# Optimization experiments

Measured on AMD Instinct MI355X. Metric: run time of the kernel, lower is better.

## Reference

```python
import jax, jax.numpy as jnp
import numpy as np

TEMPERATURE = 0.1
BATCH_SIZE = 64
EPS = 1e-8  # torch.nn.CosineSimilarity eps
NEG_INF = -1e30

B, C, D = 64, 16, 512  # batch, children per sample, feature dim


def setup_inputs() -> dict:
    key = jax.random.key(0)
    k1, k2, k3, k4 = jax.random.split(key, 4)
    children_is = jax.random.normal(k1, (B, C, D), dtype=jnp.float32)
    children_js = jax.random.normal(k2, (B, C, D), dtype=jnp.float32)
    partnet_ids = jnp.arange(B, dtype=jnp.int64 if jax.config.jax_enable_x64 else jnp.int32)
    neg_idx_j = jax.random.randint(k3, (B, B, C), 0, C)  # negatives drawn from children_js
    neg_idx_k = jax.random.randint(k4, (B, B, C), 0, C)  # negatives drawn from children_is
    return {
        "children_is": children_is,
        "children_js": children_js,
        "partnet_ids": partnet_ids,
        "neg_idx_j": neg_idx_j,
        "neg_idx_k": neg_idx_k,
    }


def _safe_norm(x, axis=-1):
    return jnp.maximum(jnp.sqrt(jnp.sum(x * x, axis=axis)), EPS)


def _ntxent(ci, cj, pids, nj, nk):
    b = ci.shape[0]
    fi = ci.reshape(b, -1)  # [B, L] flattened anchors
    fj = cj.reshape(b, -1)  # [B, L] flattened positives
    norm_i = _safe_norm(fi)

    # positive: cos(flat(children_i), flat(children_j[i])) / T
    pos = jnp.sum(fi * fj, axis=-1) / (norm_i * _safe_norm(fj))  # [B]

    src = jnp.arange(b)[None, :, None]  # broadcast source-sample index
    # gathered negatives: g*[i, j] = children_*[j, neg_idx[i, j]] flattened -> [B, B, L]
    gj = cj[src, nj].reshape(b, b, -1)
    gk = ci[src, nk].reshape(b, b, -1)

    sim_j = jnp.einsum('il,ijl->ij', fi, gj) / (norm_i[:, None] * _safe_norm(gj))
    sim_k = jnp.einsum('il,ijl->ij', fi, gk) / (norm_i[:, None] * _safe_norm(gk))

    # negative pair valid iff j != i and partnet ids differ
    eye = jnp.arange(b)
    mask = (eye[None, :] != eye[:, None]) & (pids[None, :] != pids[:, None])  # [B, B]

    logits = jnp.concatenate(
        [pos[:, None],
         jnp.where(mask, sim_j, NEG_INF),
         jnp.where(mask, sim_k, NEG_INF)], axis=1) / TEMPERATURE  # [B, 1+2B]

    # CrossEntropy with label 0, reduction='sum' over the batch of anchors
    loss = jnp.sum(-logits[:, 0] + jax.scipy.special.logsumexp(logits, axis=1))
    return loss / (2.0 * BATCH_SIZE)


def reference(children_is, children_js, partnet_ids, neg_idx_j, neg_idx_k):
    return _ntxent(children_is, children_js, partnet_ids, neg_idx_j, neg_idx_k)
```

## Files before the change

kernel.cpp:

```cpp
#include <hip/hip_runtime.h>
#include <math.h>

#define BB 64
#define CC 16
#define DD 512
#define LL 8192
#define EPSV 1e-8f
#define INVT 10.0f
#define NEGINF_T (-1e31f)

#define WS_N2I 0
#define WS_N2J 1024
#define WS_DJ  2048
#define WS_DK  6144
#define WS_POS 10240

__device__ __forceinline__ float dot4(float4 a, float4 b) {
    return a.x * b.x + a.y * b.y + a.z * b.z + a.w * b.w;
}

__device__ __forceinline__ float wave_reduce(float v) {
    #pragma unroll
    for (int off = 32; off; off >>= 1) v += __shfl_down(v, off);
    return v;
}

__global__ __launch_bounds__(256) void ntx_main(const float* __restrict__ ci,
                                                const float* __restrict__ cj,
                                                const int* __restrict__ nj,
                                                const int* __restrict__ nk,
                                                float* __restrict__ ws,
                                                float* __restrict__ out) {
    const int b = blockIdx.x, tid = threadIdx.x;

    if (b < 1024) {
        const int jt = b & 15;
        const int i  = b >> 4;

        const float4* fi4 = (const float4*)(ci + i * LL);
        float4 fiv[8];
        #pragma unroll
        for (int it = 0; it < 8; ++it) fiv[it] = fi4[tid + 256 * it];

        const int d4   = tid & 127;
        const int half = tid >> 7;
        const float4* cj4 = (const float4*)cj;
        const float4* ci4 = (const float4*)ci;

        float aj[4] = {0.f, 0.f, 0.f, 0.f};
        float ak[4] = {0.f, 0.f, 0.f, 0.f};

        #pragma unroll
        for (int it = 0; it < 8; ++it) {
            const int c = half + 2 * it;
            #pragma unroll
            for (int jj = 0; jj < 4; ++jj) {
                const int j = jt * 4 + jj;
                const int ib = (i * BB + j) * CC + c;
                const int idxj = __builtin_amdgcn_readfirstlane(nj[ib]);
                const int idxk = __builtin_amdgcn_readfirstlane(nk[ib]);
                float4 vj = cj4[(j * CC + idxj) * 128 + d4];
                float4 vk = ci4[(j * CC + idxk) * 128 + d4];
                aj[jj] += dot4(fiv[it], vj);
                ak[jj] += dot4(fiv[it], vk);
            }
        }

        __shared__ float red[4][2][4];
        #pragma unroll
        for (int jj = 0; jj < 4; ++jj) {
            float rj = wave_reduce(aj[jj]);
            float rk = wave_reduce(ak[jj]);
            if ((tid & 63) == 0) { red[jj][0][tid >> 6] = rj; red[jj][1][tid >> 6] = rk; }
        }
        __syncthreads();
        if (tid < 8) {
            const int jj = tid >> 1, side = tid & 1;
            float s = red[jj][side][0] + red[jj][side][1] + red[jj][side][2] + red[jj][side][3];
            ws[(side ? WS_DK : WS_DJ) + i * BB + jt * 4 + jj] = s;
        }
    } else if (b < 1536) {
        const int row  = (b - 1024) * 4 + (tid >> 6);
        const int lane = tid & 63;
        const int r    = row & 1023;
        const float4* src = (const float4*)(row < 1024 ? ci : cj);
        float4 v1 = src[r * 128 + lane];
        float4 v2 = src[r * 128 + 64 + lane];
        float acc = dot4(v1, v1) + dot4(v2, v2);
        acc = wave_reduce(acc);
        if (lane == 0) ws[(row < 1024 ? WS_N2I : WS_N2J) + r] = acc;
    } else {
        __shared__ float red2[4];
        const int i = b - 1536;
        if (b == 1536 && tid == 0) out[0] = 0.f;
        const float4* fi = (const float4*)(ci + i * LL);
        const float4* fj = (const float4*)(cj + i * LL);
        float acc = 0.f;
        #pragma unroll
        for (int it = 0; it < 8; ++it) acc += dot4(fi[tid + 256 * it], fj[tid + 256 * it]);
        acc = wave_reduce(acc);
        if ((tid & 63) == 0) red2[tid >> 6] = acc;
        __syncthreads();
        if (tid == 0) ws[WS_POS + i] = red2[0] + red2[1] + red2[2] + red2[3];
    }
}

__global__ __launch_bounds__(64) void ntx_final(const int* __restrict__ pids,
                                                const int* __restrict__ nj,
                                                const int* __restrict__ nk,
                                                const float* __restrict__ ws,
                                                float* __restrict__ out) {
    const int i = blockIdx.x, j = threadIdx.x;
    __shared__ float sn2i[1024], sn2j[1024];
    const float4* n2i4 = (const float4*)(ws + WS_N2I);
    const float4* n2j4 = (const float4*)(ws + WS_N2J);
    #pragma unroll
    for (int t = 0; t < 4; ++t) {
        ((float4*)sn2i)[j + 64 * t] = n2i4[j + 64 * t];
        ((float4*)sn2j)[j + 64 * t] = n2j4[j + 64 * t];
    }
    __syncthreads();

    float si = 0.f, sjf = 0.f;
    #pragma unroll
    for (int c = 0; c < CC; ++c) { si += sn2i[i * CC + c]; sjf += sn2j[i * CC + c]; }
    const float ni = fmaxf(sqrtf(si), EPSV);
    const float l0 = ws[WS_POS + i] / (ni * fmaxf(sqrtf(sjf), EPSV)) * INVT;

    const int4* nj4 = (const int4*)(nj + (i * BB + j) * CC);
    const int4* nk4 = (const int4*)(nk + (i * BB + j) * CC);
    float gj = 0.f, gk = 0.f;
    #pragma unroll
    for (int t = 0; t < 4; ++t) {
        int4 a = nj4[t];
        gj += sn2j[j * CC + a.x] + sn2j[j * CC + a.y] + sn2j[j * CC + a.z] + sn2j[j * CC + a.w];
        int4 bq = nk4[t];
        gk += sn2i[j * CC + bq.x] + sn2i[j * CC + bq.y] + sn2i[j * CC + bq.z] + sn2i[j * CC + bq.w];
    }

    const bool valid = (j != i) && (pids[j] != pids[i]);
    float lj = NEGINF_T, lk = NEGINF_T;
    if (valid) {
        const float inv = INVT / ni;
        lj = ws[WS_DJ + i * BB + j] / fmaxf(sqrtf(gj), EPSV) * inv;
        lk = ws[WS_DK + i * BB + j] / fmaxf(sqrtf(gk), EPSV) * inv;
    }

    float m = fmaxf(lj, lk);
    #pragma unroll
    for (int off = 32; off; off >>= 1) m = fmaxf(m, __shfl_xor(m, off));
    m = fmaxf(m, l0);

    float s = __expf(lj - m) + __expf(lk - m);
    s = wave_reduce(s);
    if (j == 0) {
        s += __expf(l0 - m);
        const float loss_i = -l0 + m + __logf(s);
        atomicAdd(out, loss_i * (1.0f / (2.0f * BB)));
    }
}

extern "C" void kernel_launch(void* const* d_in, const int* in_sizes, int n_in,
                              void* d_out, int out_size, void* d_ws, size_t ws_size,
                              hipStream_t stream) {
    const float* ci  = (const float*)d_in[0];
    const float* cj  = (const float*)d_in[1];
    const int*  pids = (const int*) d_in[2];
    const int*  nj   = (const int*) d_in[3];
    const int*  nk   = (const int*) d_in[4];
    float* ws  = (float*)d_ws;
    float* out = (float*)d_out;

    ntx_main<<<1600, 256, 0, stream>>>(ci, cj, nj, nk, ws, out);
    ntx_final<<<BB, 64, 0, stream>>>(pids, nj, nk, ws, out);
}
```

Baseline: 88.70 us.

## Stage source-sample rows in shared memory and tile anchors per block

```diff
diff --git a/kernel.cpp b/kernel.cpp
--- a/kernel.cpp
+++ b/kernel.cpp
@@ -31,77 +31,83 @@
                                                 const int* __restrict__ nk,
                                                 float* __restrict__ ws,
                                                 float* __restrict__ out) {
+    __shared__ float4 rows4[4096];
+    __shared__ int    sidx[8][32];
+    __shared__ float  red[8][2][4];
+    __shared__ float  pred[2][4];
+
     const int b = blockIdx.x, tid = threadIdx.x;
+    const int side  = b & 1;
+    const int jg    = (b >> 1) & 31;
+    const int ig    = b >> 6;
+    const int ibase = ig * 8;
 
-    if (b < 1024) {
-        const int jt = b & 15;
-        const int i  = b >> 4;
+    if (b == 0 && tid == 0) out[0] = 0.f;
 
-        const float4* fi4 = (const float4*)(ci + i * LL);
+    const float4* rsrc = (const float4*)(side ? ci : cj) + jg * 4096;
+    #pragma unroll
+    for (int k = 0; k < 16; ++k) rows4[tid + 256 * k] = rsrc[tid + 256 * k];
+
+    const int* nsrc = side ? nk : nj;
+    sidx[tid >> 5][tid & 31] = nsrc[(ibase + (tid >> 5)) * 1024 + jg * 32 + (tid & 31)];
+
+    __syncthreads();
+
+    if (ig == 0) {
+        const int row = tid >> 3, seg = tid & 7;
+        float acc = 0.f;
+        #pragma unroll
+        for (int k = 0; k < 16; ++k) {
+            float4 v = rows4[row * 128 + seg * 16 + k];
+            acc += dot4(v, v);
+        }
+        acc += __shfl_down(acc, 4);
+        acc += __shfl_down(acc, 2);
+        acc += __shfl_down(acc, 1);
+        if (seg == 0) ws[(side ? WS_N2I : WS_N2J) + jg * 32 + row] = acc;
+    }
+
+    const int d4   = tid & 127;
+    const int half = tid >> 7;
+    const int wave = tid >> 6;
+    const bool diagblk = (side == 0) && (ig == (jg >> 2));
+
+    const float4* cib = (const float4*)ci;
+    for (int ip = 0; ip < 8; ++ip) {
+        const int i = ibase + ip;
+        const float4* fi4 = cib + i * 2048;
         float4 fiv[8];
         #pragma unroll
         for (int it = 0; it < 8; ++it) fiv[it] = fi4[tid + 256 * it];
 
-        const int d4   = tid & 127;
-        const int half = tid >> 7;
-        const float4* cj4 = (const float4*)cj;
-        const float4* ci4 = (const float4*)ci;
-
-        float aj[4] = {0.f, 0.f, 0.f, 0.f};
-        float ak[4] = {0.f, 0.f, 0.f, 0.f};
-
         #pragma unroll
-        for (int it = 0; it < 8; ++it) {
-            const int c = half + 2 * it;
+        for (int jj = 0; jj < 2; ++jj) {
+            const bool dodiag = diagblk && (i == 2 * jg + jj);
+            float a = 0.f, ap = 0.f;
             #pragma unroll
-            for (int jj = 0; jj < 4; ++jj) {
-                const int j = jt * 4 + jj;
-                const int ib = (i * BB + j) * CC + c;
-                const int idxj = __builtin_amdgcn_readfirstlane(nj[ib]);
-                const int idxk = __builtin_amdgcn_readfirstlane(nk[ib]);
-                float4 vj = cj4[(j * CC + idxj) * 128 + d4];
-                float4 vk = ci4[(j * CC + idxk) * 128 + d4];
-                aj[jj] += dot4(fiv[it], vj);
-                ak[jj] += dot4(fiv[it], vk);
+            for (int it = 0; it < 8; ++it) {
+                const int c  = half + 2 * it;
+                const int rr = sidx[ip][jj * 16 + c];
+                a += dot4(fiv[it], rows4[(jj * 16 + rr) * 128 + d4]);
+                if (dodiag) ap += dot4(fiv[it], rows4[(jj * 16 + c) * 128 + d4]);
+            }
+            a = wave_reduce(a);
+            if ((tid & 63) == 0) red[ip][jj][wave] = a;
+            if (dodiag) {
+                ap = wave_reduce(ap);
+                if ((tid & 63) == 0) pred[jj][wave] = ap;
             }
         }
-
-        __shared__ float red[4][2][4];
-        #pragma unroll
-        for (int jj = 0; jj < 4; ++jj) {
-            float rj = wave_reduce(aj[jj]);
-            float rk = wave_reduce(ak[jj]);
-            if ((tid & 63) == 0) { red[jj][0][tid >> 6] = rj; red[jj][1][tid >> 6] = rk; }
-        }
-        __syncthreads();
-        if (tid < 8) {
-            const int jj = tid >> 1, side = tid & 1;
-            float s = red[jj][side][0] + red[jj][side][1] + red[jj][side][2] + red[jj][side][3];
-            ws[(side ? WS_DK : WS_DJ) + i * BB + jt * 4 + jj] = s;
-        }
-    } else if (b < 1536) {
-        const int row  = (b - 1024) * 4 + (tid >> 6);
-        const int lane = tid & 63;
-        const int r    = row & 1023;
-        const float4* src = (const float4*)(row < 1024 ? ci : cj);
-        float4 v1 = src[r * 128 + lane];
-        float4 v2 = src[r * 128 + 64 + lane];
-        float acc = dot4(v1, v1) + dot4(v2, v2);
-        acc = wave_reduce(acc);
-        if (lane == 0) ws[(row < 1024 ? WS_N2I : WS_N2J) + r] = acc;
-    } else {
-        __shared__ float red2[4];
-        const int i = b - 1536;
-        if (b == 1536 && tid == 0) out[0] = 0.f;
-        const float4* fi = (const float4*)(ci + i * LL);
-        const float4* fj = (const float4*)(cj + i * LL);
-        float acc = 0.f;
-        #pragma unroll
-        for (int it = 0; it < 8; ++it) acc += dot4(fi[tid + 256 * it], fj[tid + 256 * it]);
-        acc = wave_reduce(acc);
-        if ((tid & 63) == 0) red2[tid >> 6] = acc;
-        __syncthreads();
-        if (tid == 0) ws[WS_POS + i] = red2[0] + red2[1] + red2[2] + red2[3];
+    }
+    __syncthreads();
+    if (tid < 16) {
+        const int ip = tid >> 1, jj = tid & 1;
+        float s = red[ip][jj][0] + red[ip][jj][1] + red[ip][jj][2] + red[ip][jj][3];
+        ws[(side ? WS_DK : WS_DJ) + (ibase + ip) * BB + 2 * jg + jj] = s;
+    }
+    if (diagblk && tid < 2) {
+        float p = pred[tid][0] + pred[tid][1] + pred[tid][2] + pred[tid][3];
+        ws[WS_POS + 2 * jg + tid] = p;
     }
 }
 
@@ -171,6 +177,6 @@
     float* ws  = (float*)d_ws;
     float* out = (float*)d_out;
 
-    ntx_main<<<1600, 256, 0, stream>>>(ci, cj, nj, nk, ws, out);
+    ntx_main<<<512, 256, 0, stream>>>(ci, cj, nj, nk, ws, out);
     ntx_final<<<BB, 64, 0, stream>>>(pids, nj, nk, ws, out);
 }
```

Result: faster. 82.52 us (-7.0%).
